# Kernel tuning notes

Measured on AMD Instinct MI355X. Metric: run time of the kernel, lower is better.

The kernel has to match this reference:

```python
import jax, jax.numpy as jnp
import numpy as np

N, S, C, G = 40000, 16, 96, 12
EPS = 1e-5

def ln(x, g, b):
    mu = jnp.mean(x, -1, keepdims=True)
    var = jnp.mean((x - mu) ** 2, -1, keepdims=True)
    return (x - mu) * jax.lax.rsqrt(var + EPS) * g + b

def setup_inputs() -> dict:
    key = jax.random.key(0)
    ks = jax.random.split(key, 20)
    s = 0.05
    inp = {
        'q': jax.random.normal(ks[0], (N, C), jnp.float32),
        'k': jax.random.normal(ks[1], (N, C), jnp.float32),
        'v': jax.random.normal(ks[2], (N, C), jnp.float32),
        'xyz': jax.random.normal(ks[3], (N, 3), jnp.float32),
        'reference_index': jax.random.randint(ks[4], (N, S), 0, N, jnp.int32),
        # linear_q: Linear(C,C)+LN(C)+ReLU
        'Wq': jax.random.normal(ks[5], (C, C), jnp.float32) * s,
        'bq': jnp.zeros((C,), jnp.float32),
        'gq': jnp.ones((C,), jnp.float32),
        'betaq': jnp.zeros((C,), jnp.float32),
        # linear_k
        'Wk': jax.random.normal(ks[6], (C, C), jnp.float32) * s,
        'bk': jnp.zeros((C,), jnp.float32),
        'gk': jnp.ones((C,), jnp.float32),
        'betak': jnp.zeros((C,), jnp.float32),
        # linear_v
        'Wv': jax.random.normal(ks[7], (C, C), jnp.float32) * s,
        'bv': jnp.zeros((C,), jnp.float32),
        # linear_p_bias: Linear(3,C)+LN(C)+ReLU+Linear(C,C)
        'Wp1': jax.random.normal(ks[8], (3, C), jnp.float32) * s,
        'bp1': jnp.zeros((C,), jnp.float32),
        'gp': jnp.ones((C,), jnp.float32),
        'betap': jnp.zeros((C,), jnp.float32),
        'Wp2': jax.random.normal(ks[9], (C, C), jnp.float32) * s,
        'bp2': jnp.zeros((C,), jnp.float32),
        # weight_encoding: Linear(C,G)+LN(G)+ReLU+Linear(G,G)
        'Ww1': jax.random.normal(ks[10], (C, G), jnp.float32) * s,
        'bw1': jnp.zeros((G,), jnp.float32),
        'gw': jnp.ones((G,), jnp.float32),
        'betaw': jnp.zeros((G,), jnp.float32),
        'Ww2': jax.random.normal(ks[11], (G, G), jnp.float32) * s,
        'bw2': jnp.zeros((G,), jnp.float32),
    }
    return inp

def reference(q, k, v, xyz, reference_index,
              Wq, bq, gq, betaq, Wk, bk, gk, betak, Wv, bv,
              Wp1, bp1, gp, betap, Wp2, bp2,
              Ww1, bw1, gw, betaw, Ww2, bw2):
    query = jax.nn.relu(ln(q @ Wq + bq, gq, betaq))            # [N, C]
    keyf  = jax.nn.relu(ln(k @ Wk + bk, gk, betak))            # [N, C]
    val   = v @ Wv + bv                                        # [N, C]

    idx = reference_index                                      # [N, S]
    mask = (idx >= 0).astype(q.dtype)                          # sign(idx+1)
    safe = jnp.clip(idx, 0, None)
    # pointops.grouping: gather w/ zero-fill at idx=-1; with_xyz prepends relative coords
    pos  = (xyz[safe] - xyz[:, None, :]) * mask[..., None]     # [N, S, 3]
    keyg = keyf[safe] * mask[..., None]                        # [N, S, C]
    valg = val[safe] * mask[..., None]                         # [N, S, C]

    rel = keyg - query[:, None, :]                             # [N, S, C]
    peb = jax.nn.relu(ln(pos @ Wp1 + bp1, gp, betap)) @ Wp2 + bp2
    rel = rel + peb
    valg = valg + peb

    w = jax.nn.relu(ln(rel @ Ww1 + bw1, gw, betaw)) @ Ww2 + bw2  # [N, S, G]
    w = jax.nn.softmax(w, axis=1) * mask[..., None]              # softmax over neighbors

    valg = valg.reshape(N, S, G, C // G)
    feat = jnp.einsum('nsgi,nsg->ngi', valg, w).reshape(N, C)
    return feat
```

## Files before the change

### kernel.cpp

```cpp
#include <hip/hip_runtime.h>

#define NN 40000
#define SS 16
#define CC 96
#define GG 12
#define SXP 104

typedef __attribute__((ext_vector_type(8))) short bf16x8;
typedef __attribute__((ext_vector_type(4))) float f32x4;

__device__ __forceinline__ short f2bf(float f) {
    union { float f; unsigned u; } c; c.f = f;
    unsigned r = (c.u + 0x7fffu + ((c.u >> 16) & 1u)) >> 16;
    return (short)r;
}
__device__ __forceinline__ unsigned pack2bf(float hi, float lo) {
    unsigned a = __float_as_uint(hi) + 0x8000u;
    unsigned b = __float_as_uint(lo) + 0x8000u;
    return __builtin_amdgcn_perm(a, b, 0x07060302u);
}
__device__ __forceinline__ ushort f2bf_hu(float f) {
    return (ushort)((__float_as_uint(f) + 0x8000u) >> 16);
}

template<int CTRL>
__device__ __forceinline__ float dppf(float x) {
    int r = __builtin_amdgcn_mov_dpp(__float_as_int(x), CTRL, 0xF, 0xF, true);
    return __int_as_float(r);
}
__device__ __forceinline__ float row16_sum(float x) {
    x += dppf<0xB1>(x);
    x += dppf<0x4E>(x);
    x += dppf<0x141>(x);
    x += dppf<0x140>(x);
    return x;
}
__device__ __forceinline__ float row16_max(float x) {
    x = fmaxf(x, dppf<0xB1>(x));
    x = fmaxf(x, dppf<0x4E>(x));
    x = fmaxf(x, dppf<0x141>(x));
    x = fmaxf(x, dppf<0x140>(x));
    return x;
}

#define J_W3   27648
#define J_P2   (J_W3 + 9216)
#define J_W1   (J_P2 + 1536)
#define J_WF   (J_W1 + 1536)
#define J_CF   (J_WF + 12)
#define J_S4   (J_CF + 4)
#define J_G    (J_S4 + 16)

__global__ void prep_kernel(const float* __restrict__ Wq, const float* __restrict__ Wk,
                            const float* __restrict__ Wv, const float* __restrict__ Wp2,
                            const float* __restrict__ Ww1, const float* __restrict__ bp2,
                            const float* __restrict__ bw1, const float* __restrict__ Wp1,
                            const float* __restrict__ bp1,
                            ushort* __restrict__ fragQKV, ushort* __restrict__ fragP2,
                            ushort* __restrict__ fragW1, ushort* __restrict__ fragWf,
                            float* __restrict__ cfused, float* __restrict__ stats)
{
    const int job = blockIdx.x*256 + threadIdx.x;
    if (job < J_W3) {
        const int which = job / 9216, o = job % 9216;
        const float* W = (which == 0) ? Wq : (which == 1) ? Wk : Wv;
        const int pos = o >> 3, j = o & 7;
        const int lane = pos & 63, ntkb = pos >> 6;
        const int nt = ntkb / 3, kb = ntkb - nt*3;
        const int col = nt*16 + (lane & 15), krow = kb*32 + (lane >> 4)*8 + j;
        fragQKV[job] = (ushort)f2bf(W[krow*CC + col]);
    } else if (job < J_P2) {
        const int o = job - J_W3;
        const int pos = o >> 3, j = o & 7;
        const int lane = pos & 63, ntkb = pos >> 6;
        const int nt = ntkb / 3, kb = ntkb - nt*3;
        const int col = nt*16 + (lane & 15), krow = kb*32 + (lane >> 4)*8 + j;
        fragP2[o] = (ushort)f2bf(Wp2[krow*CC + col]);
    } else if (job < J_W1) {
        const int o = job - J_P2;
        const int pos = o >> 3, j = o & 7;
        const int lane = pos & 63, kb = pos >> 6;
        const int col = lane & 15, krow = kb*32 + (lane >> 4)*8 + j;
        fragW1[o] = (col < GG) ? (ushort)f2bf(Ww1[krow*GG + col]) : (ushort)0;
    } else if (job < J_WF) {
        const int o = job - J_W1;
        const int pos = o >> 3, j = o & 7;
        const int lane = pos & 63, kb = pos >> 6;
        const int col = lane & 15, krow = kb*32 + (lane >> 4)*8 + j;
        float s = 0.f;
        if (col < GG) for (int jj = 0; jj < CC; ++jj) s += Wp2[krow*CC + jj] * Ww1[jj*GG + col];
        fragWf[o] = (col < GG) ? (ushort)f2bf(s) : (ushort)0;
    } else if (job < J_CF) {
        const int g = job - J_WF;
        float s = bw1[g];
        for (int jj = 0; jj < CC; ++jj) s += bp2[jj] * Ww1[jj*GG + g];
        cfused[g] = s;
    } else if (job < J_S4) {
        const int d = job - J_CF;
        float s = 0.f;
        for (int c = 0; c < CC; ++c) s += (d < 3) ? Wp1[d*CC + c] : bp1[c];
        stats[d] = s;
    } else if (job < J_G) {
        const int o = job - J_S4, d1 = o >> 2, d2 = o & 3;
        float s = 0.f;
        for (int c = 0; c < CC; ++c) {
            const float a1 = (d1 < 3) ? Wp1[d1*CC + c] : bp1[c];
            const float a2 = (d2 < 3) ? Wp1[d2*CC + c] : bp1[c];
            s += a1*a2;
        }
        stats[4 + o] = s;
    }
}

__global__ __launch_bounds__(256) void qkv_mfma(
    const float* __restrict__ q, const float* __restrict__ kx, const float* __restrict__ v,
    const float* __restrict__ bq, const float* __restrict__ gq, const float* __restrict__ betaq,
    const float* __restrict__ bk, const float* __restrict__ gk, const float* __restrict__ betak,
    const float* __restrict__ bv,
    const ushort* __restrict__ fragQKV, const ushort* __restrict__ fragW1,
    float* __restrict__ valout, float* __restrict__ qw1out, float* __restrict__ kw1out)
{
    __shared__ float sbias[CC], sg[CC], sbeta[CC];
    __shared__ __align__(16) ushort sx2[4][16*SXP];

    const int p = blockIdx.y;
    const float* X; const float* b;
    const float* g = nullptr; const float* beta = nullptr;
    if (p == 0)      { X = q;  b = bq; g = gq; beta = betaq; }
    else if (p == 1) { X = kx; b = bk; g = gk; beta = betak; }
    else             { X = v;  b = bv; }
    const bool has_ln = (p < 2);
    float* w1out = (p == 0) ? qw1out : kw1out;

    const int t = threadIdx.x;
    if (t < CC) {
        sbias[t] = b[t];
        if (has_ln) { sg[t] = g[t]; sbeta[t] = beta[t]; }
    }

    const int lane = t & 63, w = t >> 6;
    const int c16 = lane & 15, quad = lane >> 4;
    const ushort* fragW = fragQKV + p*9216;

    bf16x8 Ww1f[3];
    if (has_ln) {
        #pragma unroll
        for (int kb = 0; kb < 3; ++kb) {
            union { bf16x8 v; uint4 u; } wu;
            wu.u = ((const uint4*)fragW1)[kb*64 + lane];
            Ww1f[kb] = wu.v;
        }
    }

    __syncthreads();

    const f32x4 zero4 = {0.f, 0.f, 0.f, 0.f};
    ushort* sxw = sx2[w];
    const int tile = blockIdx.x*4 + w;
    const int row0 = tile * 16;

    const float* xr = X + (size_t)(row0 + c16)*CC;
    bf16x8 Af[3];
    #pragma unroll
    for (int kb = 0; kb < 3; ++kb) {
        const float4 a0 = *(const float4*)(xr + kb*32 + quad*8);
        const float4 a1 = *(const float4*)(xr + kb*32 + quad*8 + 4);
        union { bf16x8 v; uint u[4]; } au;
        au.u[0] = pack2bf(a0.y, a0.x);
        au.u[1] = pack2bf(a0.w, a0.z);
        au.u[2] = pack2bf(a1.y, a1.x);
        au.u[3] = pack2bf(a1.w, a1.z);
        Af[kb] = au.v;
    }

    f32x4 acc[6];
    #pragma unroll
    for (int nt = 0; nt < 6; ++nt) acc[nt] = zero4;
    #pragma unroll
    for (int kb = 0; kb < 3; ++kb)
        #pragma unroll
        for (int nt = 0; nt < 6; ++nt) {
            const bf16x8 bf = *(const bf16x8*)(fragW + ((nt*3 + kb)*64 + lane)*8);
            acc[nt] = __builtin_amdgcn_mfma_f32_16x16x32_bf16(Af[kb], bf, acc[nt], 0, 0, 0);
        }

    #pragma unroll
    for (int nt = 0; nt < 6; ++nt) {
        const float bb = sbias[nt*16 + c16];
        #pragma unroll
        for (int r = 0; r < 4; ++r) acc[nt][r] += bb;
    }

    if (has_ln) {
        #pragma unroll
        for (int r = 0; r < 4; ++r) {
            float sum = 0.f, sq = 0.f;
            #pragma unroll
            for (int nt = 0; nt < 6; ++nt) { float x = acc[nt][r]; sum += x; sq += x*x; }
            sum = row16_sum(sum); sq = row16_sum(sq);
            const float mu  = sum * (1.f/96.f);
            const float var = sq * (1.f/96.f) - mu*mu;
            const float rs  = rsqrtf(var + 1e-5f);
            #pragma unroll
            for (int nt = 0; nt < 6; ++nt) {
                const int c = nt*16 + c16;
                acc[nt][r] = fmaxf((acc[nt][r] - mu)*rs*sg[c] + sbeta[c], 0.f);
            }
        }
        #pragma unroll
        for (int nt = 0; nt < 6; ++nt)
            #pragma unroll
            for (int r = 0; r < 4; ++r)
                sxw[(quad*4 + r)*SXP + nt*16 + c16] = f2bf_hu(acc[nt][r]);

        f32x4 o = zero4;
        #pragma unroll
        for (int kb = 0; kb < 3; ++kb) {
            const bf16x8 aA = *(const bf16x8*)(sxw + c16*SXP + kb*32 + quad*8);
            o = __builtin_amdgcn_mfma_f32_16x16x32_bf16(aA, Ww1f[kb], o, 0, 0, 0);
        }
        if (c16 < GG) {
            #pragma unroll
            for (int r = 0; r < 4; ++r)
                w1out[(size_t)(row0 + quad*4 + r)*GG + c16] = o[r];
        }
    } else {
        #pragma unroll
        for (int r = 0; r < 4; ++r)
            #pragma unroll
            for (int nt = 0; nt < 6; ++nt)
                valout[(size_t)(row0 + quad*4 + r)*CC + nt*16 + c16] = acc[nt][r];
    }
}

__global__ __launch_bounds__(256) void attn2(
    const float* __restrict__ xyz, const int* __restrict__ refidx,
    const float* __restrict__ gp,  const float* __restrict__ betap,
    const float* __restrict__ Wp1, const float* __restrict__ bp1,
    const float* __restrict__ bp2,
    const float* __restrict__ gw,  const float* __restrict__ betaw,
    const float* __restrict__ Ww2, const float* __restrict__ bw2,
    const float* __restrict__ cfused, const float* __restrict__ stats,
    const ushort* __restrict__ fragP2, const ushort* __restrict__ fragWf,
    const float* __restrict__ valw, const float* __restrict__ kw1w, const float* __restrict__ qw1w,
    float* __restrict__ out)
{
    __shared__ __align__(16) ushort sWp2f[9216];
    __shared__ float4 sA[CC];
    __shared__ float2 sGB[CC];
    __shared__ float  sbp2[CC];
    __shared__ __align__(16) float sWw2T[GG*GG];
    __shared__ float  sgw[16], sbetaw[16], sbw2[16], scf[16];
    __shared__ float  sstats[20];
    __shared__ __align__(16) float ybuf[4][2][SS*GG];

    const int t = threadIdx.x;
    if (t < CC) {
        sA[t]  = make_float4(Wp1[t], Wp1[CC + t], Wp1[2*CC + t], bp1[t]);
        sGB[t] = make_float2(gp[t], betap[t]);
        sbp2[t] = bp2[t];
    }
    if (t < GG*GG) {
        const int gr = t / GG, gc = t - gr*GG;
        sWw2T[gc*GG + gr] = Ww2[t];
    }
    if (t < 16) {
        sgw[t]    = (t < GG) ? gw[t]     : 0.f;
        sbetaw[t] = (t < GG) ? betaw[t]  : 0.f;
        sbw2[t]   = (t < GG) ? bw2[t]    : 0.f;
        scf[t]    = (t < GG) ? cfused[t] : 0.f;
    }
    if (t < 20) sstats[t] = stats[t];
    for (int i = t; i < 1152; i += 256) ((uint4*)sWp2f)[i] = ((const uint4*)fragP2)[i];

    const int lane = t & 63, w = t >> 6;
    const int c16 = lane & 15, quad = lane >> 4;
    const int gcl = (c16 < GG) ? c16 : (GG-1);
    const float laneg = (c16 < GG) ? 1.f : 0.f;

    __syncthreads();

    const f32x4 zero4 = {0.f, 0.f, 0.f, 0.f};
    const int n0 = blockIdx.x*8 + w*2;

    int   id[2];  int4 rr[2];
    #pragma unroll
    for (int u = 0; u < 2; ++u) {
        id[u] = refidx[(size_t)(n0 + u)*SS + c16];
        rr[u] = *(const int4*)(refidx + (size_t)(n0 + u)*SS + quad*4);
    }

    float mm[2], px[2], py[2], pz[2];
    #pragma unroll
    for (int u = 0; u < 2; ++u) {
        mm[u] = (id[u] >= 0) ? 1.f : 0.f;
        const int safe = (id[u] < 0) ? 0 : id[u];
        const int nn = n0 + u;
        px[u] = (xyz[(size_t)safe*3 + 0] - xyz[(size_t)nn*3 + 0]) * mm[u];
        py[u] = (xyz[(size_t)safe*3 + 1] - xyz[(size_t)nn*3 + 1]) * mm[u];
        pz[u] = (xyz[(size_t)safe*3 + 2] - xyz[(size_t)nn*3 + 2]) * mm[u];
    }

    int sid[2][4]; float mrg[2][4];
    #pragma unroll
    for (int u = 0; u < 2; ++u) {
        const int rv0 = rr[u].x, rv1 = rr[u].y, rv2 = rr[u].z, rv3 = rr[u].w;
        sid[u][0] = (rv0 < 0) ? 0 : rv0;  mrg[u][0] = (rv0 >= 0) ? laneg : 0.f;
        sid[u][1] = (rv1 < 0) ? 0 : rv1;  mrg[u][1] = (rv1 >= 0) ? laneg : 0.f;
        sid[u][2] = (rv2 < 0) ? 0 : rv2;  mrg[u][2] = (rv2 >= 0) ? laneg : 0.f;
        sid[u][3] = (rv3 < 0) ? 0 : rv3;  mrg[u][3] = (rv3 >= 0) ? laneg : 0.f;
    }

    float kwr[2][4], qvl[2];
    #pragma unroll
    for (int u = 0; u < 2; ++u) {
        #pragma unroll
        for (int r = 0; r < 4; ++r)
            kwr[u][r] = kw1w[(size_t)sid[u][r]*GG + gcl];
        qvl[u] = qw1w[(size_t)(n0 + u)*GG + gcl];
    }

    float va[2][3][2][4];
    #pragma unroll
    for (int u = 0; u < 2; ++u)
        #pragma unroll
        for (int ntp = 0; ntp < 3; ++ntp)
            #pragma unroll
            for (int h = 0; h < 2; ++h)
                #pragma unroll
                for (int r = 0; r < 4; ++r)
                    va[u][ntp][h][r] = valw[(size_t)sid[u][r]*CC + (2*ntp + h)*16 + c16];

    bf16x8 Wff[3];
    #pragma unroll
    for (int kb = 0; kb < 3; ++kb) {
        union { bf16x8 v; uint4 u; } wu;
        wu.u = ((const uint4*)fragWf)[kb*64 + lane];
        Wff[kb] = wu.v;
    }

    __builtin_amdgcn_sched_barrier(0);

    float muv[2], rsv[2];
    {
        const float s0 = sstats[0], s1 = sstats[1], s2 = sstats[2], s3 = sstats[3];
        float G_[16];
        #pragma unroll
        for (int i = 0; i < 16; ++i) G_[i] = sstats[4 + i];
        #pragma unroll
        for (int u = 0; u < 2; ++u) {
            muv[u] = (px[u]*s0 + py[u]*s1 + pz[u]*s2 + s3) * (1.f/96.f);
            const float p4[4] = {px[u], py[u], pz[u], 1.f};
            float e2 = 0.f;
            #pragma unroll
            for (int a = 0; a < 4; ++a) {
                float ta = 0.f;
                #pragma unroll
                for (int b2 = 0; b2 < 4; ++b2) ta = fmaf(G_[a*4 + b2], p4[b2], ta);
                e2 = fmaf(p4[a], ta, e2);
            }
            const float var = e2*(1.f/96.f) - muv[u]*muv[u];
            rsv[u] = rsqrtf(var + 1e-5f);
        }
    }

    bf16x8 t1A[2][3];
    #pragma unroll
    for (int kb = 0; kb < 3; ++kb) {
        uint tw[2][4];
        #pragma unroll
        for (int jp = 0; jp < 4; ++jp) {
            const int c0 = kb*32 + quad*8 + jp*2, c1 = c0 + 1;
            const float4 aw0 = sA[c0], aw1 = sA[c1];
            const float2 gb0 = sGB[c0], gb1 = sGB[c1];
            #pragma unroll
            for (int u = 0; u < 2; ++u) {
                const float x0 = fmaf(px[u], aw0.x, fmaf(py[u], aw0.y, fmaf(pz[u], aw0.z, aw0.w)));
                const float x1 = fmaf(px[u], aw1.x, fmaf(py[u], aw1.y, fmaf(pz[u], aw1.z, aw1.w)));
                const float t0 = fmaxf(fmaf((x0 - muv[u])*rsv[u], gb0.x, gb0.y), 0.f);
                const float t1v = fmaxf(fmaf((x1 - muv[u])*rsv[u], gb1.x, gb1.y), 0.f);
                tw[u][jp] = pack2bf(t1v, t0);
            }
        }
        #pragma unroll
        for (int u = 0; u < 2; ++u) {
            union { bf16x8 v; uint uu[4]; } tc;
            tc.uu[0] = tw[u][0]; tc.uu[1] = tw[u][1];
            tc.uu[2] = tw[u][2]; tc.uu[3] = tw[u][3];
            t1A[u][kb] = tc.v;
        }
    }

    f32x4 t2[2];
    #pragma unroll
    for (int u = 0; u < 2; ++u) t2[u] = zero4;
    #pragma unroll
    for (int kb = 0; kb < 3; ++kb)
        #pragma unroll
        for (int u = 0; u < 2; ++u)
            t2[u] = __builtin_amdgcn_mfma_f32_16x16x32_bf16(t1A[u][kb], Wff[kb], t2[u], 0, 0, 0);
    {
        const float cf = scf[c16];
        #pragma unroll
        for (int u = 0; u < 2; ++u) {
            const float qz = qvl[u]*laneg;
            #pragma unroll
            for (int r = 0; r < 4; ++r)
                t2[u][r] += kwr[u][r]*mrg[u][r] - qz + cf;
        }
    }

    {
        const float gwv = sgw[c16], bwv = sbetaw[c16];
        #pragma unroll
        for (int u = 0; u < 2; ++u) {
            float* yb = ybuf[w][u];
            #pragma unroll
            for (int r = 0; r < 4; ++r) {
                const float x = t2[u][r];
                const float s1 = row16_sum(x);
                const float s2 = row16_sum(x*x);
                const float mu2  = s1 * (1.f/12.f);
                const float var2 = s2 * (1.f/12.f) - mu2*mu2;
                const float rs2  = rsqrtf(var2 + 1e-5f);
                const float y    = fmaxf((x - mu2)*rs2*gwv + bwv, 0.f);
                if (c16 < GG) yb[(quad*4 + r)*GG + c16] = y;
            }
        }
    }

    float w3v[2][3];
    {
        f32x4 yr[2][3];
        #pragma unroll
        for (int u = 0; u < 2; ++u) {
            yr[u][0] = *(const f32x4*)(ybuf[w][u] + c16*GG + 0);
            yr[u][1] = *(const f32x4*)(ybuf[w][u] + c16*GG + 4);
            yr[u][2] = *(const f32x4*)(ybuf[w][u] + c16*GG + 8);
        }
        #pragma unroll
        for (int gi = 0; gi < 3; ++gi) {
            const int gpp = quad + gi*4;
            const f32x4 wa = *(const f32x4*)(sWw2T + gpp*GG + 0);
            const f32x4 wb = *(const f32x4*)(sWw2T + gpp*GG + 4);
            const f32x4 wc = *(const f32x4*)(sWw2T + gpp*GG + 8);
            const float bb = sbw2[gpp];
            #pragma unroll
            for (int u = 0; u < 2; ++u) {
                float a2 = bb;
                #pragma unroll
                for (int j = 0; j < 4; ++j) a2 = fmaf(yr[u][0][j], wa[j], a2);
                #pragma unroll
                for (int j = 0; j < 4; ++j) a2 = fmaf(yr[u][1][j], wb[j], a2);
                #pragma unroll
                for (int j = 0; j < 4; ++j) a2 = fmaf(yr[u][2][j], wc[j], a2);
                w3v[u][gi] = a2;
            }
        }
    }

    #pragma unroll
    for (int u = 0; u < 2; ++u) {
        #pragma unroll
        for (int gi = 0; gi < 3; ++gi) {
            const float mx = row16_max(w3v[u][gi]);
            const float e  = __expf(w3v[u][gi] - mx);
            const float tot = row16_sum(e);
            w3v[u][gi] = e * __builtin_amdgcn_rcpf(tot) * mm[u];
        }
        float* sw2 = ybuf[w][u];
        #pragma unroll
        for (int gi = 0; gi < 3; ++gi)
            sw2[(quad + 4*gi)*16 + c16] = w3v[u][gi];
    }

    #pragma unroll
    for (int ntp = 0; ntp < 3; ++ntp) {
        const int nt0 = 2*ntp, nt1 = 2*ntp + 1;
        f32x4 pa[2], pb[2];
        #pragma unroll
        for (int u = 0; u < 2; ++u) { pa[u] = zero4; pb[u] = zero4; }
        #pragma unroll
        for (int kb = 0; kb < 3; ++kb) {
            const bf16x8 bfa = *(const bf16x8*)(sWp2f + ((nt0*3 + kb)*64 + lane)*8);
            const bf16x8 bfb = *(const bf16x8*)(sWp2f + ((nt1*3 + kb)*64 + lane)*8);
            #pragma unroll
            for (int u = 0; u < 2; ++u) {
                pa[u] = __builtin_amdgcn_mfma_f32_16x16x32_bf16(t1A[u][kb], bfa, pa[u], 0, 0, 0);
                pb[u] = __builtin_amdgcn_mfma_f32_16x16x32_bf16(t1A[u][kb], bfb, pb[u], 0, 0, 0);
            }
        }
        #pragma unroll
        for (int h = 0; h < 2; ++h) {
            const int nt = 2*ntp + h;
            const float b2   = sbp2[nt*16 + c16];
            const int   gidx = 2*nt + (c16 >> 3);
            #pragma unroll
            for (int u = 0; u < 2; ++u) {
                const f32x4 pc  = (h == 0) ? pa[u] : pb[u];
                const f32x4 swv = *(const f32x4*)(ybuf[w][u] + gidx*16 + quad*4);
                float a2 = 0.f;
                #pragma unroll
                for (int r = 0; r < 4; ++r)
                    a2 = fmaf(pc[r] + b2 + va[u][ntp][h][r], swv[r], a2);
                a2 += __shfl_xor(a2, 16, 64);
                a2 += __shfl_xor(a2, 32, 64);
                if (quad == 0) out[(size_t)(n0 + u)*CC + nt*16 + c16] = a2;
            }
        }
    }
}

extern "C" void kernel_launch(void* const* d_in, const int* in_sizes, int n_in,
                              void* d_out, int out_size, void* d_ws, size_t ws_size,
                              hipStream_t stream)
{
    const float* q     = (const float*)d_in[0];
    const float* k     = (const float*)d_in[1];
    const float* v     = (const float*)d_in[2];
    const float* xyz   = (const float*)d_in[3];
    const int*   ridx  = (const int*)d_in[4];
    const float* Wq    = (const float*)d_in[5];
    const float* bq    = (const float*)d_in[6];
    const float* gq    = (const float*)d_in[7];
    const float* betaq = (const float*)d_in[8];
    const float* Wk    = (const float*)d_in[9];
    const float* bk    = (const float*)d_in[10];
    const float* gk    = (const float*)d_in[11];
    const float* betak = (const float*)d_in[12];
    const float* Wv    = (const float*)d_in[13];
    const float* bv    = (const float*)d_in[14];
    const float* Wp1   = (const float*)d_in[15];
    const float* bp1   = (const float*)d_in[16];
    const float* gp    = (const float*)d_in[17];
    const float* betap = (const float*)d_in[18];
    const float* Wp2   = (const float*)d_in[19];
    const float* bp2   = (const float*)d_in[20];
    const float* Ww1   = (const float*)d_in[21];
    const float* bw1   = (const float*)d_in[22];
    const float* gw    = (const float*)d_in[23];
    const float* betaw = (const float*)d_in[24];
    const float* Ww2   = (const float*)d_in[25];
    const float* bw2   = (const float*)d_in[26];
    float* out = (float*)d_out;

    float* ws = (float*)d_ws;
    float* valw   = ws;
    float* kw1w   = valw + (size_t)NN*CC;
    float* qw1w   = kw1w + (size_t)NN*GG;
    float* cfused = qw1w + (size_t)NN*GG;
    float* statsp = cfused + 16;
    ushort* fragQKV = (ushort*)(statsp + 24);
    ushort* fragP2  = fragQKV + 3*9216;
    ushort* fragW1  = fragP2 + 9216;
    ushort* fragWf  = fragW1 + 1536;

    prep_kernel<<<dim3(157, 1, 1), 256, 0, stream>>>(
        Wq, Wk, Wv, Wp2, Ww1, bp2, bw1, Wp1, bp1,
        fragQKV, fragP2, fragW1, fragWf, cfused, statsp);

    qkv_mfma<<<dim3(625, 3, 1), 256, 0, stream>>>(
        q, k, v, bq, gq, betaq, bk, gk, betak, bv,
        fragQKV, fragW1, valw, qw1w, kw1w);

    attn2<<<dim3(5000, 1, 1), 256, 0, stream>>>(
        xyz, ridx, gp, betap, Wp1, bp1, bp2,
        gw, betaw, Ww2, bw2, cfused, statsp,
        fragP2, fragWf, valw, kw1w, qw1w, out);
}
```

Measured before the change: 214.5 us.

## Pack value and key-weight features into interleaved bf16 rows for gathers

```diff
diff --git a/kernel.cpp b/kernel.cpp
--- a/kernel.cpp
+++ b/kernel.cpp
@@ -4,6 +4,7 @@
 #define SS 16
 #define CC 96
 #define GG 12
+#define VKS 128
 #define SXP 104
 
 typedef __attribute__((ext_vector_type(8))) short bf16x8;
@@ -21,6 +22,9 @@
 }
 __device__ __forceinline__ ushort f2bf_hu(float f) {
     return (ushort)((__float_as_uint(f) + 0x8000u) >> 16);
+}
+__device__ __forceinline__ float bf2f(ushort u) {
+    return __uint_as_float(((unsigned)u) << 16);
 }
 
 template<int CTRL>
@@ -116,23 +120,29 @@
     const float* __restrict__ q, const float* __restrict__ kx, const float* __restrict__ v,
     const float* __restrict__ bq, const float* __restrict__ gq, const float* __restrict__ betaq,
     const float* __restrict__ bk, const float* __restrict__ gk, const float* __restrict__ betak,
-    const float* __restrict__ bv,
+    const float* __restrict__ bv, const float* __restrict__ xyz,
     const ushort* __restrict__ fragQKV, const ushort* __restrict__ fragW1,
-    float* __restrict__ valout, float* __restrict__ qw1out, float* __restrict__ kw1out)
+    ushort* __restrict__ vkp, ushort* __restrict__ qw1out, float* __restrict__ xyzp)
 {
+    const int p = blockIdx.y;
+    const int t = threadIdx.x;
+
+    if (p == 3) {
+        const int rrow = blockIdx.x*64 + (t >> 2), c = t & 3;
+        xyzp[(size_t)rrow*4 + c] = (c < 3) ? xyz[(size_t)rrow*3 + c] : 0.f;
+        return;
+    }
+
     __shared__ float sbias[CC], sg[CC], sbeta[CC];
     __shared__ __align__(16) ushort sx2[4][16*SXP];
 
-    const int p = blockIdx.y;
     const float* X; const float* b;
     const float* g = nullptr; const float* beta = nullptr;
     if (p == 0)      { X = q;  b = bq; g = gq; beta = betaq; }
     else if (p == 1) { X = kx; b = bk; g = gk; beta = betak; }
     else             { X = v;  b = bv; }
     const bool has_ln = (p < 2);
-    float* w1out = (p == 0) ? qw1out : kw1out;
-
-    const int t = threadIdx.x;
+
     if (t < CC) {
         sbias[t] = b[t];
         if (has_ln) { sg[t] = g[t]; sbeta[t] = beta[t]; }
@@ -221,20 +231,27 @@
         }
         if (c16 < GG) {
             #pragma unroll
-            for (int r = 0; r < 4; ++r)
-                w1out[(size_t)(row0 + quad*4 + r)*GG + c16] = o[r];
+            for (int r = 0; r < 4; ++r) {
+                if (p == 0)
+                    qw1out[(size_t)(row0 + quad*4 + r)*GG + c16] = (ushort)f2bf(o[r]);
+                else
+                    vkp[(size_t)(row0 + quad*4 + r)*VKS + c16*8 + 6] = (ushort)f2bf(o[r]);
+            }
         }
     } else {
         #pragma unroll
-        for (int r = 0; r < 4; ++r)
-            #pragma unroll
-            for (int nt = 0; nt < 6; ++nt)
-                valout[(size_t)(row0 + quad*4 + r)*CC + nt*16 + c16] = acc[nt][r];
+        for (int r = 0; r < 4; ++r) {
+            ushort* dst = vkp + (size_t)(row0 + quad*4 + r)*VKS + c16*8;
+            #pragma unroll
+            for (int nt = 0; nt < 6; ++nt) dst[nt] = (ushort)f2bf(acc[nt][r]);
+            dst[7] = 0;
+            if (c16 >= GG) dst[6] = 0;
+        }
     }
 }
 
 __global__ __launch_bounds__(256) void attn2(
-    const float* __restrict__ xyz, const int* __restrict__ refidx,
+    const float4* __restrict__ xyzp, const int* __restrict__ refidx,
     const float* __restrict__ gp,  const float* __restrict__ betap,
     const float* __restrict__ Wp1, const float* __restrict__ bp1,
     const float* __restrict__ bp2,
@@ -242,7 +259,7 @@
     const float* __restrict__ Ww2, const float* __restrict__ bw2,
     const float* __restrict__ cfused, const float* __restrict__ stats,
     const ushort* __restrict__ fragP2, const ushort* __restrict__ fragWf,
-    const float* __restrict__ valw, const float* __restrict__ kw1w, const float* __restrict__ qw1w,
+    const ushort* __restrict__ vkp, const ushort* __restrict__ qw1w,
     float* __restrict__ out)
 {
     __shared__ __align__(16) ushort sWp2f[9216];
@@ -289,48 +306,12 @@
         id[u] = refidx[(size_t)(n0 + u)*SS + c16];
         rr[u] = *(const int4*)(refidx + (size_t)(n0 + u)*SS + quad*4);
     }
-
-    float mm[2], px[2], py[2], pz[2];
-    #pragma unroll
-    for (int u = 0; u < 2; ++u) {
-        mm[u] = (id[u] >= 0) ? 1.f : 0.f;
-        const int safe = (id[u] < 0) ? 0 : id[u];
-        const int nn = n0 + u;
-        px[u] = (xyz[(size_t)safe*3 + 0] - xyz[(size_t)nn*3 + 0]) * mm[u];
-        py[u] = (xyz[(size_t)safe*3 + 1] - xyz[(size_t)nn*3 + 1]) * mm[u];
-        pz[u] = (xyz[(size_t)safe*3 + 2] - xyz[(size_t)nn*3 + 2]) * mm[u];
-    }
-
-    int sid[2][4]; float mrg[2][4];
-    #pragma unroll
-    for (int u = 0; u < 2; ++u) {
-        const int rv0 = rr[u].x, rv1 = rr[u].y, rv2 = rr[u].z, rv3 = rr[u].w;
-        sid[u][0] = (rv0 < 0) ? 0 : rv0;  mrg[u][0] = (rv0 >= 0) ? laneg : 0.f;
-        sid[u][1] = (rv1 < 0) ? 0 : rv1;  mrg[u][1] = (rv1 >= 0) ? laneg : 0.f;
-        sid[u][2] = (rv2 < 0) ? 0 : rv2;  mrg[u][2] = (rv2 >= 0) ? laneg : 0.f;
-        sid[u][3] = (rv3 < 0) ? 0 : rv3;  mrg[u][3] = (rv3 >= 0) ? laneg : 0.f;
-    }
-
-    float kwr[2][4], qvl[2];
-    #pragma unroll
-    for (int u = 0; u < 2; ++u) {
-        #pragma unroll
-        for (int r = 0; r < 4; ++r)
-            kwr[u][r] = kw1w[(size_t)sid[u][r]*GG + gcl];
-        qvl[u] = qw1w[(size_t)(n0 + u)*GG + gcl];
-    }
-
-    float va[2][3][2][4];
-    #pragma unroll
-    for (int u = 0; u < 2; ++u)
-        #pragma unroll
-        for (int ntp = 0; ntp < 3; ++ntp)
-            #pragma unroll
-            for (int h = 0; h < 2; ++h)
-                #pragma unroll
-                for (int r = 0; r < 4; ++r)
-                    va[u][ntp][h][r] = valw[(size_t)sid[u][r]*CC + (2*ntp + h)*16 + c16];
-
+    ushort qvu[2];
+    #pragma unroll
+    for (int u = 0; u < 2; ++u) qvu[u] = qw1w[(size_t)(n0 + u)*GG + gcl];
+    float4 cx[2];
+    #pragma unroll
+    for (int u = 0; u < 2; ++u) cx[u] = xyzp[n0 + u];
     bf16x8 Wff[3];
     #pragma unroll
     for (int kb = 0; kb < 3; ++kb) {
@@ -339,7 +320,41 @@
         Wff[kb] = wu.v;
     }
 
+    float mm[2]; int safe1[2];
+    #pragma unroll
+    for (int u = 0; u < 2; ++u) {
+        mm[u]    = (id[u] >= 0) ? 1.f : 0.f;
+        safe1[u] = (id[u] < 0) ? 0 : id[u];
+    }
+    int sid[2][4]; float mrg[2][4];
+    #pragma unroll
+    for (int u = 0; u < 2; ++u) {
+        const int rv0 = rr[u].x, rv1 = rr[u].y, rv2 = rr[u].z, rv3 = rr[u].w;
+        sid[u][0] = (rv0 < 0) ? 0 : rv0;  mrg[u][0] = (rv0 >= 0) ? 1.f : 0.f;
+        sid[u][1] = (rv1 < 0) ? 0 : rv1;  mrg[u][1] = (rv1 >= 0) ? 1.f : 0.f;
+        sid[u][2] = (rv2 < 0) ? 0 : rv2;  mrg[u][2] = (rv2 >= 0) ? 1.f : 0.f;
+        sid[u][3] = (rv3 < 0) ? 0 : rv3;  mrg[u][3] = (rv3 >= 0) ? 1.f : 0.f;
+    }
+
+    float4 sx[2];
+    #pragma unroll
+    for (int u = 0; u < 2; ++u) sx[u] = xyzp[safe1[u]];
+    bf16x8 vk[2][4];
+    #pragma unroll
+    for (int u = 0; u < 2; ++u)
+        #pragma unroll
+        for (int r = 0; r < 4; ++r)
+            vk[u][r] = *(const bf16x8*)(vkp + (size_t)sid[u][r]*VKS + c16*8);
+
     __builtin_amdgcn_sched_barrier(0);
+
+    float px[2], py[2], pz[2];
+    #pragma unroll
+    for (int u = 0; u < 2; ++u) {
+        px[u] = (sx[u].x - cx[u].x) * mm[u];
+        py[u] = (sx[u].y - cx[u].y) * mm[u];
+        pz[u] = (sx[u].z - cx[u].z) * mm[u];
+    }
 
     float muv[2], rsv[2];
     {
@@ -403,10 +418,10 @@
         const float cf = scf[c16];
         #pragma unroll
         for (int u = 0; u < 2; ++u) {
-            const float qz = qvl[u]*laneg;
+            const float qz = bf2f(qvu[u])*laneg;
             #pragma unroll
             for (int r = 0; r < 4; ++r)
-                t2[u][r] += kwr[u][r]*mrg[u][r] - qz + cf;
+                t2[u][r] += bf2f((ushort)vk[u][r][6])*mrg[u][r] - qz + cf;
         }
     }
 
@@ -502,7 +517,7 @@
                 float a2 = 0.f;
                 #pragma unroll
                 for (int r = 0; r < 4; ++r)
-                    a2 = fmaf(pc[r] + b2 + va[u][ntp][h][r], swv[r], a2);
+                    a2 = fmaf(pc[r] + b2 + bf2f((ushort)vk[u][r][nt]), swv[r], a2);
                 a2 += __shfl_xor(a2, 16, 64);
                 a2 += __shfl_xor(a2, 32, 64);
                 if (quad == 0) out[(size_t)(n0 + u)*CC + nt*16 + c16] = a2;
@@ -544,11 +559,10 @@
     const float* bw2   = (const float*)d_in[26];
     float* out = (float*)d_out;
 
-    float* ws = (float*)d_ws;
-    float* valw   = ws;
-    float* kw1w   = valw + (size_t)NN*CC;
-    float* qw1w   = kw1w + (size_t)NN*GG;
-    float* cfused = qw1w + (size_t)NN*GG;
+    ushort* vkp   = (ushort*)d_ws;
+    ushort* qw1w  = vkp + (size_t)NN*VKS;
+    float*  xyzp  = (float*)(qw1w + (size_t)NN*GG);
+    float* cfused = xyzp + (size_t)NN*4;
     float* statsp = cfused + 16;
     ushort* fragQKV = (ushort*)(statsp + 24);
     ushort* fragP2  = fragQKV + 3*9216;
@@ -559,12 +573,12 @@
         Wq, Wk, Wv, Wp2, Ww1, bp2, bw1, Wp1, bp1,
         fragQKV, fragP2, fragW1, fragWf, cfused, statsp);
 
-    qkv_mfma<<<dim3(625, 3, 1), 256, 0, stream>>>(
-        q, k, v, bq, gq, betaq, bk, gk, betak, bv,
-        fragQKV, fragW1, valw, qw1w, kw1w);
+    qkv_mfma<<<dim3(625, 4, 1), 256, 0, stream>>>(
+        q, k, v, bq, gq, betaq, bk, gk, betak, bv, xyz,
+        fragQKV, fragW1, vkp, qw1w, xyzp);
 
     attn2<<<dim3(5000, 1, 1), 256, 0, stream>>>(
-        xyz, ridx, gp, betap, Wp1, bp1, bp2,
+        (const float4*)xyzp, ridx, gp, betap, Wp1, bp1, bp2,
         gw, betaw, Ww2, bw2, cfused, statsp,
-        fragP2, fragWf, valw, kw1w, qw1w, out);
-}
+        fragP2, fragWf, vkp, qw1w, out);
+}
```

Result: faster. 206.9 us, median of 2 (-3.6%).
